# Optimization experiments

Measured on AMD Instinct MI355X. Metric: run time of the kernel, lower is better.

Reference implementation:

```python
import jax, jax.numpy as jnp
import numpy as np

IN, SD, PD, K = 34, 4, 22, 8
WIDTH, NUM_CLASSES, NCONV = 126, 6, 2
N, NGRAPH = 16384, 8
BATCH_OFFSET = 1e3  # separates graphs in learned coordinate space
BLOCK = 1024


def knn_idx(s, k, block=BLOCK):
    # brute-force kNN in blocks of query rows; s: [N, SD]
    n = s.shape[0]
    rows = s.reshape(n // block, block, s.shape[-1])
    def f(r):  # r: [block, SD]
        d2 = jnp.sum((r[:, None, :] - s[None, :, :]) ** 2, -1)  # [block, N]
        _, idx = jax.lax.top_k(-d2, k)
        return idx
    return jax.lax.map(f, rows).reshape(n, k)


def gravnet_conv(x, batch, Ws, bs, Wh, bh, Wo1, Wo2, bo2):
    # s: learned coordinates, offset per-graph so kNN never crosses graphs
    s = x @ Ws + bs + (batch.astype(x.dtype) * BATCH_OFFSET)[:, None]  # [N, SD]
    h = x @ Wh + bh                                                    # [N, PD]
    idx = knn_idx(jax.lax.stop_gradient(s), K)                         # [N, K]
    d2 = jnp.sum((s[:, None, :] - s[idx]) ** 2, -1)                    # [N, K]
    w = jnp.exp(-10.0 * d2)                                            # [N, K]
    msg = h[idx] * w[..., None]                                        # [N, K, PD]
    agg = jnp.concatenate([msg.mean(1), msg.max(1)], -1)               # [N, 2*PD]
    return x @ Wo1 + agg @ Wo2 + bo2                                   # [N, IN]


def setup_inputs() -> dict:
    key = jax.random.key(0)
    ks = jax.random.split(key, 12)
    def g(k, shape, fan_in):
        return jax.random.normal(k, shape, jnp.float32) * (fan_in ** -0.5)
    return {
        "x": jax.random.normal(ks[0], (N, IN), jnp.float32),
        "batch": jnp.sort(jax.random.randint(ks[1], (N,), 0, NGRAPH)),
        "Ws": g(ks[2], (NCONV, IN, SD), IN),
        "bs": jnp.zeros((NCONV, SD), jnp.float32),
        "Wh": g(ks[3], (NCONV, IN, PD), IN),
        "bh": jnp.zeros((NCONV, PD), jnp.float32),
        "Wo1": g(ks[4], (NCONV, IN, IN), IN),
        "Wo2": g(ks[5], (NCONV, 2 * PD, IN), 2 * PD),
        "bo2": jnp.zeros((NCONV, IN), jnp.float32),
        "W1": g(ks[6], (IN, WIDTH), IN),
        "b1": jnp.zeros((WIDTH,), jnp.float32),
        "W2": g(ks[7], (WIDTH, WIDTH), WIDTH),
        "b2": jnp.zeros((WIDTH,), jnp.float32),
        "W3": g(ks[8], (WIDTH, NUM_CLASSES), WIDTH),
        "b3": jnp.zeros((NUM_CLASSES,), jnp.float32),
    }


def reference(x, batch, Ws, bs, Wh, bh, Wo1, Wo2, bo2, W1, b1, W2, b2, W3, b3):
    # Faithful to original: input_ is never updated, each conv sees raw x,
    # only the last conv's embedding feeds the MLP head.
    embedding = x
    for i in range(NCONV):
        embedding = gravnet_conv(x, batch, Ws[i], bs[i], Wh[i], bh[i], Wo1[i], Wo2[i], bo2[i])
    hdd = jax.nn.elu(embedding @ W1 + b1)
    hdd = jax.nn.elu(hdd @ W2 + b2)
    return hdd @ W3 + b3  # [N, NUM_CLASSES]
```

## Files before the change

kernel.cpp:

```cpp
#include <hip/hip_runtime.h>
#include <math.h>
#include <float.h>

#define NPT     16384
#define IN_F    34
#define SDIM    4
#define PDIM    22
#define KNN     8
#define WIDTH   126
#define WPAD    128
#define NCLS    6
#define ROWS    32

typedef unsigned long long u64;

#define OFF_RANGES 0
#define OFF_S      256
#define OFF_H      (OFF_S  + NPT*SDIM*4)
#define OFF_KIDX   (OFF_H  + NPT*PDIM*4)
#define OFF_KW     (OFF_KIDX + NPT*KNN*4)

#define INITK_BITS 0x7f7fffffffffffffULL

__device__ __forceinline__ void ce(double& a, double& b) {
    double mn = __builtin_fmin(a, b);
    double mx = __builtin_fmax(a, b);
    a = mn; b = mx;
}
__device__ __forceinline__ double dmin64(double a, double b) {
    return __builtin_fmin(a, b);
}
__device__ __forceinline__ double pack_key(float d2, unsigned j) {
    return __longlong_as_double((long long)(((u64)__float_as_uint(d2) << 32) | j));
}

__device__ __forceinline__ void key_insert(double key, double* u) {
#pragma unroll
    for (int t = 0; t < KNN; ++t) {
        double mn = __builtin_fmin(key, u[t]);
        double mx = __builtin_fmax(key, u[t]);
        u[t] = mn;
        key  = mx;
    }
}

__device__ __forceinline__ void lgkm_barrier() {
    asm volatile("s_waitcnt lgkmcnt(0)" ::: "memory");
    __builtin_amdgcn_s_barrier();
    asm volatile("" ::: "memory");
}

__device__ __forceinline__ float dist2(const float4 a, const float4 b) {
    float d0 = a.x - b.x;
    float d1 = a.y - b.y;
    float d2 = a.z - b.z;
    float d3 = a.w - b.w;
    return __fadd_rn(__fadd_rn(__fadd_rn(__fmul_rn(d0, d0),
                                         __fmul_rn(d1, d1)),
                               __fmul_rn(d2, d2)),
                     __fmul_rn(d3, d3));
}

#define BITONIC8(m0,m1,m2,m3,m4,m5,m6,m7) \
    ce(m0,m4); ce(m1,m5); ce(m2,m6); ce(m3,m7); \
    ce(m0,m2); ce(m1,m3); ce(m4,m6); ce(m5,m7); \
    ce(m0,m1); ce(m2,m3); ce(m4,m5); ce(m6,m7);

#define SORT8(k0,k1,k2,k3,k4,k5,k6,k7) \
    ce(k0,k1); ce(k2,k3); ce(k4,k5); ce(k6,k7); \
    ce(k0,k2); ce(k1,k3); ce(k4,k6); ce(k5,k7); \
    ce(k1,k2); ce(k5,k6); \
    ce(k0,k4); ce(k1,k5); ce(k2,k6); ce(k3,k7); \
    ce(k2,k4); ce(k3,k5); \
    ce(k1,k2); ce(k3,k4); ce(k5,k6);

__global__ __launch_bounds__(256) void k_sh(const float* __restrict__ x,
                                            const int* __restrict__ batch,
                                            const float* __restrict__ Ws,
                                            const float* __restrict__ bs,
                                            const float* __restrict__ Wh,
                                            const float* __restrict__ bh,
                                            float* __restrict__ S,
                                            float* __restrict__ H,
                                            int* __restrict__ ranges) {
    int t = blockIdx.x * blockDim.x + threadIdx.x;
    int i = t >> 5;
    int o = t & 31;
    if (i >= NPT) return;
    if (o == 31) {
        int b = batch[i];
        if (i == 0 || batch[i - 1] != b) ranges[b * 2]     = i;
        if (i == NPT - 1 || batch[i + 1] != b) ranges[b * 2 + 1] = i + 1;
        return;
    }
    const float* xr = x + (size_t)i * IN_F;
    if (o < SDIM) {
        float acc = 0.f;
        for (int k = 0; k < IN_F; ++k) acc += xr[k] * Ws[k * SDIM + o];
        S[(size_t)i * SDIM + o] = (acc + bs[o]) + 1000.f * (float)batch[i];
    } else if (o < SDIM + PDIM) {
        int p = o - SDIM;
        float acc = 0.f;
        for (int k = 0; k < IN_F; ++k) acc += xr[k] * Wh[k * PDIM + p];
        H[(size_t)i * PDIM + p] = acc + bh[p];
    }
}

__global__ __launch_bounds__(256, 4) void k_knn(const float4* __restrict__ S4,
                                                const int* __restrict__ batch,
                                                const int* __restrict__ ranges,
                                                int* __restrict__ KIDX,
                                                float* __restrict__ KW) {
    const int tid = threadIdx.x;
    const int q   = blockIdx.x * 8 + (tid >> 5);
    const int t   = tid & 31;
    const int b   = batch[q];
    const int gs  = ranges[b * 2];
    const int len = ranges[b * 2 + 1] - gs;
    const float4 sq = S4[q];

    double u[KNN];
    const double initk = __longlong_as_double((long long)INITK_BITS);
#pragma unroll
    for (int e = 0; e < KNN; ++e) u[e] = initk;

    int j = gs + t;
    int done = 0;

    const int nfull8 = len >> 8;
    for (int bb = 0; bb < nfull8; ++bb, j += 256) {
        const float4* p = S4 + j;
        float4 s0 = p[0];
        float4 s1 = p[32];
        float4 s2 = p[64];
        float4 s3 = p[96];
        float4 s4 = p[128];
        float4 s5 = p[160];
        float4 s6 = p[192];
        float4 s7 = p[224];
        double k0 = pack_key(dist2(sq, s0), (unsigned)(j));
        double k1 = pack_key(dist2(sq, s1), (unsigned)(j + 32));
        double k2 = pack_key(dist2(sq, s2), (unsigned)(j + 64));
        double k3 = pack_key(dist2(sq, s3), (unsigned)(j + 96));
        double k4 = pack_key(dist2(sq, s4), (unsigned)(j + 128));
        double k5 = pack_key(dist2(sq, s5), (unsigned)(j + 160));
        double k6 = pack_key(dist2(sq, s6), (unsigned)(j + 192));
        double k7 = pack_key(dist2(sq, s7), (unsigned)(j + 224));
        SORT8(k0, k1, k2, k3, k4, k5, k6, k7);
        double m0 = dmin64(k0, u[7]);
        double m1 = dmin64(k1, u[6]);
        double m2 = dmin64(k2, u[5]);
        double m3 = dmin64(k3, u[4]);
        double m4 = dmin64(k4, u[3]);
        double m5 = dmin64(k5, u[2]);
        double m6 = dmin64(k6, u[1]);
        double m7 = dmin64(k7, u[0]);
        BITONIC8(m0, m1, m2, m3, m4, m5, m6, m7);
        u[0] = m0; u[1] = m1; u[2] = m2; u[3] = m3;
        u[4] = m4; u[5] = m5; u[6] = m6; u[7] = m7;
    }
    done = nfull8 << 8;

    if (len - done >= 128) {
        const float4* p = S4 + j;
        float4 s0 = p[0];
        float4 s1 = p[32];
        float4 s2 = p[64];
        float4 s3 = p[96];
        double k0 = pack_key(dist2(sq, s0), (unsigned)(j));
        double k1 = pack_key(dist2(sq, s1), (unsigned)(j + 32));
        double k2 = pack_key(dist2(sq, s2), (unsigned)(j + 64));
        double k3 = pack_key(dist2(sq, s3), (unsigned)(j + 96));
        ce(k0, k1); ce(k2, k3); ce(k0, k2); ce(k1, k3); ce(k1, k2);
        double m0 = dmin64(k0, u[7]);
        double m1 = dmin64(k1, u[6]);
        double m2 = dmin64(k2, u[5]);
        double m3 = dmin64(k3, u[4]);
        double m4 = u[3], m5 = u[2], m6 = u[1], m7 = u[0];
        BITONIC8(m0, m1, m2, m3, m4, m5, m6, m7);
        u[0] = m0; u[1] = m1; u[2] = m2; u[3] = m3;
        u[4] = m4; u[5] = m5; u[6] = m6; u[7] = m7;
        done += 128;
    }

    for (int m = done + t; m < len; m += 32) {
        int jj = gs + m;
        key_insert(pack_key(dist2(sq, S4[jj]), (unsigned)jj), u);
    }

#pragma unroll
    for (int mm = 1; mm < 32; mm <<= 1) {
        double p0 = __shfl_xor(u[0], mm, 32);
        double p1 = __shfl_xor(u[1], mm, 32);
        double p2 = __shfl_xor(u[2], mm, 32);
        double p3 = __shfl_xor(u[3], mm, 32);
        double p4 = __shfl_xor(u[4], mm, 32);
        double p5 = __shfl_xor(u[5], mm, 32);
        double p6 = __shfl_xor(u[6], mm, 32);
        double p7 = __shfl_xor(u[7], mm, 32);
        double m0 = dmin64(u[0], p7);
        double m1 = dmin64(u[1], p6);
        double m2 = dmin64(u[2], p5);
        double m3 = dmin64(u[3], p4);
        double m4 = dmin64(u[4], p3);
        double m5 = dmin64(u[5], p2);
        double m6 = dmin64(u[6], p1);
        double m7 = dmin64(u[7], p0);
        BITONIC8(m0, m1, m2, m3, m4, m5, m6, m7);
        u[0] = m0; u[1] = m1; u[2] = m2; u[3] = m3;
        u[4] = m4; u[5] = m5; u[6] = m6; u[7] = m7;
    }

    if (t == 0) {
#pragma unroll
        for (int e = 0; e < KNN; ++e) {
            u64 bits = (u64)__double_as_longlong(u[e]);
            float d = __uint_as_float((unsigned)(bits >> 32));
            KIDX[(size_t)q * KNN + e] = (int)(unsigned)(bits & 0xffffffffu);
            KW[(size_t)q * KNN + e]   = expf(-10.f * d);
        }
    }
}

__global__ __launch_bounds__(512, 4) void k_fused(
        const float* __restrict__ x,
        const float* __restrict__ H,
        const int* __restrict__ KIDX,
        const float* __restrict__ KW,
        const float* __restrict__ Wo1,
        const float* __restrict__ Wo2,
        const float* __restrict__ bo2,
        const float* __restrict__ W1,
        const float* __restrict__ b1,
        const float* __restrict__ W2,
        const float* __restrict__ b2,
        const float* __restrict__ W3,
        const float* __restrict__ b3,
        float* __restrict__ out) {
    __shared__ float xt[ROWS * IN_F];
    __shared__ float aggt[ROWS * 2 * PDIM];
    __shared__ float et[ROWS * IN_F];
    __shared__ float h1t[ROWS * WPAD];
    __shared__ float wbuf[2 * 32 * WPAD];
    __shared__ float w3buf[WPAD * NCLS];

    const int tid  = threadIdx.x;
    const int r    = tid >> 4;
    const int c    = tid & 15;
    const int p    = tid >> 5;
    const int cg   = tid & 31;
    const int row0 = blockIdx.x * ROWS;
    const int gi   = row0 + r;
    const int rA   = 2 * p;
    const int rB   = 2 * p + 1;
    const int jc   = 4 * cg;

    for (int t = tid; t < ROWS * IN_F; t += 512)
        xt[t] = x[(size_t)row0 * IN_F + t];
    for (int t = tid; t < IN_F * WPAD; t += 512) {
        int k = t >> 7, j = t & 127;
        wbuf[(k >> 5) * (32 * WPAD) + (k & 31) * WPAD + j] =
            (j < WIDTH) ? W1[k * WIDTH + j] : 0.f;
    }
    for (int t = tid; t < WPAD * NCLS; t += 512) {
        int k = t / NCLS;
        w3buf[t] = (k < WIDTH) ? W3[t] : 0.f;
    }

    if (c < 11) {
        const int p0 = c, p1 = c + 11;
        float s0 = 0.f, s1 = 0.f;
        float m0 = -FLT_MAX, m1 = -FLT_MAX;
#pragma unroll
        for (int k = 0; k < KNN; ++k) {
            int   j = KIDX[(size_t)gi * KNN + k];
            float w = KW[(size_t)gi * KNN + k];
            const float* hr = H + (size_t)j * PDIM;
            float v0 = hr[p0] * w; s0 += v0; m0 = fmaxf(m0, v0);
            float v1 = hr[p1] * w; s1 += v1; m1 = fmaxf(m1, v1);
        }
        aggt[r * 44 + p0] = s0 * 0.125f; aggt[r * 44 + PDIM + p0] = m0;
        aggt[r * 44 + p1] = s1 * 0.125f; aggt[r * 44 + PDIM + p1] = m1;
    }
    lgkm_barrier();

    float rvA[8], rvB[8];
#pragma unroll
    for (int i = 0; i < 8; ++i) {
        int e = i * 512 + tid, kk = e >> 7, j = e & 127;
        rvA[i] = (j < WIDTH) ? W2[(size_t)kk * WIDTH + j] : 0.f;
    }

    {
        const int j0 = (3 * c < 31) ? 3 * c : 31;
        float acc[3] = {0.f, 0.f, 0.f};
        const float* ar = xt + r * IN_F;
#pragma unroll 4
        for (int k = 0; k < IN_F; ++k) {
            float av = ar[k];
            const float* wr = Wo1 + k * IN_F + j0;
#pragma unroll
            for (int jj = 0; jj < 3; ++jj) acc[jj] += av * wr[jj];
        }
        const float* gr = aggt + r * 44;
#pragma unroll 4
        for (int pp = 0; pp < 2 * PDIM; ++pp) {
            float av = gr[pp];
            const float* wr = Wo2 + pp * IN_F + j0;
#pragma unroll
            for (int jj = 0; jj < 3; ++jj) acc[jj] += av * wr[jj];
        }
#pragma unroll
        for (int jj = 0; jj < 3; ++jj)
            et[r * IN_F + j0 + jj] = acc[jj] + bo2[j0 + jj];
    }
    lgkm_barrier();

    {
        float a0[4] = {0.f, 0.f, 0.f, 0.f};
        float a1[4] = {0.f, 0.f, 0.f, 0.f};
        const float* e0 = et + rA * IN_F;
        const float* e1 = et + rB * IN_F;
#pragma unroll 4
        for (int k = 0; k < IN_F; ++k) {
            const float* wr = wbuf + (k >> 5) * (32 * WPAD) + (k & 31) * WPAD;
            const float4 w4 = *(const float4*)(wr + jc);
            float v0 = e0[k], v1 = e1[k];
            a0[0] += v0 * w4.x; a0[1] += v0 * w4.y;
            a0[2] += v0 * w4.z; a0[3] += v0 * w4.w;
            a1[0] += v1 * w4.x; a1[1] += v1 * w4.y;
            a1[2] += v1 * w4.z; a1[3] += v1 * w4.w;
        }
#pragma unroll
        for (int jj = 0; jj < 4; ++jj) {
            int j = jc + jj;
            float bj = b1[j < WIDTH ? j : WIDTH - 1];
            float v0 = a0[jj] + bj;
            float v1 = a1[jj] + bj;
            h1t[rA * WPAD + j] = (j < WIDTH) ? (v0 > 0.f ? v0 : expm1f(v0)) : 0.f;
            h1t[rB * WPAD + j] = (j < WIDTH) ? (v1 > 0.f ? v1 : expm1f(v1)) : 0.f;
        }
    }
    lgkm_barrier();

    float a0[4] = {0.f, 0.f, 0.f, 0.f};
    float a1[4] = {0.f, 0.f, 0.f, 0.f};
    const float* h0 = h1t + rA * WPAD;
    const float* h1r = h1t + rB * WPAD;

#define STORE_CHUNK(BUFI, RV)                                   \
    _Pragma("unroll")                                           \
    for (int i = 0; i < 8; ++i)                                 \
        wbuf[(BUFI) * 4096 + i * 512 + tid] = RV[i];

#define LOAD_CHUNK(RV, K0)                                      \
    _Pragma("unroll")                                           \
    for (int i = 0; i < 8; ++i) {                               \
        int e = i * 512 + tid, kk = e >> 7, j = e & 127;        \
        int row = (K0) + kk;                                    \
        RV[i] = (j < WIDTH && row < WIDTH)                      \
                    ? W2[(size_t)row * WIDTH + j] : 0.f;        \
    }

#define COMPUTE_CHUNK(BUFI, K0)                                 \
    {                                                           \
        const float* wb = wbuf + (BUFI) * 4096;                 \
        _Pragma("unroll 4")                                     \
        for (int k = 0; k < 32; ++k) {                          \
            const float4 w4 = *(const float4*)(wb + k * WPAD + jc); \
            float v0 = h0[(K0) + k];                            \
            float v1 = h1r[(K0) + k];                           \
            a0[0] += v0 * w4.x; a0[1] += v0 * w4.y;             \
            a0[2] += v0 * w4.z; a0[3] += v0 * w4.w;             \
            a1[0] += v1 * w4.x; a1[1] += v1 * w4.y;             \
            a1[2] += v1 * w4.z; a1[3] += v1 * w4.w;             \
        }                                                       \
    }

    STORE_CHUNK(0, rvA);  LOAD_CHUNK(rvB, 32);
    lgkm_barrier();
    COMPUTE_CHUNK(0, 0);
    STORE_CHUNK(1, rvB);  LOAD_CHUNK(rvA, 64);
    lgkm_barrier();
    COMPUTE_CHUNK(1, 32);
    STORE_CHUNK(0, rvA);  LOAD_CHUNK(rvB, 96);
    lgkm_barrier();
    COMPUTE_CHUNK(0, 64);
    STORE_CHUNK(1, rvB);
    lgkm_barrier();
    COMPUTE_CHUNK(1, 96);

    {
        float pc0[NCLS] = {0.f, 0.f, 0.f, 0.f, 0.f, 0.f};
        float pc1[NCLS] = {0.f, 0.f, 0.f, 0.f, 0.f, 0.f};
#pragma unroll
        for (int jj = 0; jj < 4; ++jj) {
            int j = jc + jj;
            float bj = b2[j < WIDTH ? j : WIDTH - 1];
            float v0 = a0[jj] + bj;
            float v1 = a1[jj] + bj;
            float g0 = (j < WIDTH) ? (v0 > 0.f ? v0 : expm1f(v0)) : 0.f;
            float g1 = (j < WIDTH) ? (v1 > 0.f ? v1 : expm1f(v1)) : 0.f;
            const float* w3r = w3buf + j * NCLS;
#pragma unroll
            for (int cc = 0; cc < NCLS; ++cc) {
                pc0[cc] += g0 * w3r[cc];
                pc1[cc] += g1 * w3r[cc];
            }
        }
#pragma unroll
        for (int mm = 1; mm < 32; mm <<= 1) {
#pragma unroll
            for (int cc = 0; cc < NCLS; ++cc) {
                pc0[cc] += __shfl_xor(pc0[cc], mm, 32);
                pc1[cc] += __shfl_xor(pc1[cc], mm, 32);
            }
        }
        if (cg == 0) {
#pragma unroll
            for (int cc = 0; cc < NCLS; ++cc) {
                out[(size_t)(row0 + rA) * NCLS + cc] = pc0[cc] + b3[cc];
                out[(size_t)(row0 + rB) * NCLS + cc] = pc1[cc] + b3[cc];
            }
        }
    }
#undef STORE_CHUNK
#undef LOAD_CHUNK
#undef COMPUTE_CHUNK
}

extern "C" void kernel_launch(void* const* d_in, const int* in_sizes, int n_in,
                              void* d_out, int out_size, void* d_ws, size_t ws_size,
                              hipStream_t stream) {
    const float* x     = (const float*)d_in[0];
    const int*   batch = (const int*)d_in[1];
    const float* Ws  = (const float*)d_in[2] + IN_F * SDIM;
    const float* bs  = (const float*)d_in[3] + SDIM;
    const float* Wh  = (const float*)d_in[4] + IN_F * PDIM;
    const float* bh  = (const float*)d_in[5] + PDIM;
    const float* Wo1 = (const float*)d_in[6] + IN_F * IN_F;
    const float* Wo2 = (const float*)d_in[7] + 2 * PDIM * IN_F;
    const float* bo2 = (const float*)d_in[8] + IN_F;
    const float* W1  = (const float*)d_in[9];
    const float* b1  = (const float*)d_in[10];
    const float* W2  = (const float*)d_in[11];
    const float* b2  = (const float*)d_in[12];
    const float* W3  = (const float*)d_in[13];
    const float* b3  = (const float*)d_in[14];
    float* out = (float*)d_out;

    char* ws = (char*)d_ws;
    int*   ranges = (int*)(ws + OFF_RANGES);
    float* S      = (float*)(ws + OFF_S);
    float* H      = (float*)(ws + OFF_H);
    int*   KIDX   = (int*)(ws + OFF_KIDX);
    float* KW     = (float*)(ws + OFF_KW);

    k_sh<<<dim3(NPT * 32 / 256), dim3(256), 0, stream>>>(x, batch, Ws, bs, Wh, bh, S, H, ranges);
    k_knn<<<dim3(NPT / 8), dim3(256), 0, stream>>>((const float4*)S, batch, ranges, KIDX, KW);
    k_fused<<<dim3(NPT / ROWS), dim3(512), 0, stream>>>(x, H, KIDX, KW, Wo1, Wo2, bo2,
                                                        W1, b1, W2, b2, W3, b3, out);
}
```

Baseline: 76.13 us.

## Stage all MLP weights in LDS once per block and loop over two row tiles

The fused head kernel now loads W1, the full W2, Wo1, Wo2 and W3 into shared memory once per block and processes 64 rows as two 32-row tiles. This replaces the chunked double-buffered W2 streaming, and Wo1/Wo2 are no longer read from global memory inside the inner loops. Blocks are remapped with a swizzled index and launch bounds drop to one block per CU, because shared memory use grows to roughly 100KB. The aim is to amortise weight loading across more rows, at the cost of fewer blocks and lower occupancy.

```diff
diff --git a/kernel.cpp b/kernel.cpp
--- a/kernel.cpp
+++ b/kernel.cpp
@@ -10,7 +10,8 @@
 #define WIDTH   126
 #define WPAD    128
 #define NCLS    6
-#define ROWS    32
+#define RPB     64
+#define TROWS   32
 
 typedef unsigned long long u64;
 
@@ -42,12 +43,6 @@
         u[t] = mn;
         key  = mx;
     }
-}
-
-__device__ __forceinline__ void lgkm_barrier() {
-    asm volatile("s_waitcnt lgkmcnt(0)" ::: "memory");
-    __builtin_amdgcn_s_barrier();
-    asm volatile("" ::: "memory");
 }
 
 __device__ __forceinline__ float dist2(const float4 a, const float4 b) {
@@ -222,7 +217,7 @@
     }
 }
 
-__global__ __launch_bounds__(512, 4) void k_fused(
+__global__ __launch_bounds__(512, 1) void k_fused(
         const float* __restrict__ x,
         const float* __restrict__ H,
         const int* __restrict__ KIDX,
@@ -237,196 +232,169 @@
         const float* __restrict__ W3,
         const float* __restrict__ b3,
         float* __restrict__ out) {
-    __shared__ float xt[ROWS * IN_F];
-    __shared__ float aggt[ROWS * 2 * PDIM];
-    __shared__ float et[ROWS * IN_F];
-    __shared__ float h1t[ROWS * WPAD];
-    __shared__ float wbuf[2 * 32 * WPAD];
+    __shared__ float W1L[IN_F * WPAD];
+    __shared__ float W2L[WPAD * WPAD];
+    __shared__ float wo1L[IN_F * IN_F];
+    __shared__ float wo2L[2 * PDIM * IN_F];
     __shared__ float w3buf[WPAD * NCLS];
-
-    const int tid  = threadIdx.x;
-    const int r    = tid >> 4;
-    const int c    = tid & 15;
-    const int p    = tid >> 5;
-    const int cg   = tid & 31;
-    const int row0 = blockIdx.x * ROWS;
-    const int gi   = row0 + r;
-    const int rA   = 2 * p;
-    const int rB   = 2 * p + 1;
-    const int jc   = 4 * cg;
-
-    for (int t = tid; t < ROWS * IN_F; t += 512)
-        xt[t] = x[(size_t)row0 * IN_F + t];
+    __shared__ float xt[TROWS * IN_F];
+    __shared__ float aggt[TROWS * 2 * PDIM];
+    __shared__ float et[TROWS * IN_F];
+    __shared__ float h1t[TROWS * WPAD];
+
+    const int tid = threadIdx.x;
+    const int r   = tid >> 4;
+    const int c   = tid & 15;
+    const int p   = tid >> 5;
+    const int cg  = tid & 31;
+    const int rA  = 2 * p;
+    const int rB  = 2 * p + 1;
+    const int jc  = 4 * cg;
+    const int lb   = ((blockIdx.x & 7) << 5) | (blockIdx.x >> 3);
+    const int brow = lb * RPB;
+
     for (int t = tid; t < IN_F * WPAD; t += 512) {
         int k = t >> 7, j = t & 127;
-        wbuf[(k >> 5) * (32 * WPAD) + (k & 31) * WPAD + j] =
-            (j < WIDTH) ? W1[k * WIDTH + j] : 0.f;
-    }
+        W1L[t] = (j < WIDTH) ? W1[k * WIDTH + j] : 0.f;
+    }
+    for (int t = tid; t < WPAD * WPAD; t += 512) {
+        int k = t >> 7, j = t & 127;
+        W2L[t] = (k < WIDTH && j < WIDTH) ? W2[(size_t)k * WIDTH + j] : 0.f;
+    }
+    for (int t = tid; t < IN_F * IN_F; t += 512)      wo1L[t] = Wo1[t];
+    for (int t = tid; t < 2 * PDIM * IN_F; t += 512)  wo2L[t] = Wo2[t];
     for (int t = tid; t < WPAD * NCLS; t += 512) {
         int k = t / NCLS;
         w3buf[t] = (k < WIDTH) ? W3[t] : 0.f;
     }
-
-    if (c < 11) {
-        const int p0 = c, p1 = c + 11;
-        float s0 = 0.f, s1 = 0.f;
-        float m0 = -FLT_MAX, m1 = -FLT_MAX;
-#pragma unroll
-        for (int k = 0; k < KNN; ++k) {
-            int   j = KIDX[(size_t)gi * KNN + k];
-            float w = KW[(size_t)gi * KNN + k];
-            const float* hr = H + (size_t)j * PDIM;
-            float v0 = hr[p0] * w; s0 += v0; m0 = fmaxf(m0, v0);
-            float v1 = hr[p1] * w; s1 += v1; m1 = fmaxf(m1, v1);
+    __syncthreads();
+
+#pragma unroll 1
+    for (int tile = 0; tile < RPB / TROWS; ++tile) {
+        const int row0 = brow + tile * TROWS;
+        const int gi   = row0 + r;
+
+        for (int t = tid; t < TROWS * IN_F; t += 512)
+            xt[t] = x[(size_t)row0 * IN_F + t];
+        if (c < 11) {
+            const int p0 = c, p1 = c + 11;
+            float s0 = 0.f, s1 = 0.f;
+            float m0 = -FLT_MAX, m1 = -FLT_MAX;
+#pragma unroll
+            for (int k = 0; k < KNN; ++k) {
+                int   j = KIDX[(size_t)gi * KNN + k];
+                float w = KW[(size_t)gi * KNN + k];
+                const float* hr = H + (size_t)j * PDIM;
+                float v0 = hr[p0] * w; s0 += v0; m0 = fmaxf(m0, v0);
+                float v1 = hr[p1] * w; s1 += v1; m1 = fmaxf(m1, v1);
+            }
+            aggt[r * 44 + p0] = s0 * 0.125f; aggt[r * 44 + PDIM + p0] = m0;
+            aggt[r * 44 + p1] = s1 * 0.125f; aggt[r * 44 + PDIM + p1] = m1;
         }
-        aggt[r * 44 + p0] = s0 * 0.125f; aggt[r * 44 + PDIM + p0] = m0;
-        aggt[r * 44 + p1] = s1 * 0.125f; aggt[r * 44 + PDIM + p1] = m1;
-    }
-    lgkm_barrier();
-
-    float rvA[8], rvB[8];
-#pragma unroll
-    for (int i = 0; i < 8; ++i) {
-        int e = i * 512 + tid, kk = e >> 7, j = e & 127;
-        rvA[i] = (j < WIDTH) ? W2[(size_t)kk * WIDTH + j] : 0.f;
-    }
-
-    {
-        const int j0 = (3 * c < 31) ? 3 * c : 31;
-        float acc[3] = {0.f, 0.f, 0.f};
-        const float* ar = xt + r * IN_F;
+        __syncthreads();
+
+        {
+            const int j0 = (3 * c < 31) ? 3 * c : 31;
+            float acc[3] = {0.f, 0.f, 0.f};
+            const float* ar = xt + r * IN_F;
 #pragma unroll 4
-        for (int k = 0; k < IN_F; ++k) {
-            float av = ar[k];
-            const float* wr = Wo1 + k * IN_F + j0;
-#pragma unroll
-            for (int jj = 0; jj < 3; ++jj) acc[jj] += av * wr[jj];
+            for (int k = 0; k < IN_F; ++k) {
+                float av = ar[k];
+                const float* wr = wo1L + k * IN_F + j0;
+#pragma unroll
+                for (int jj = 0; jj < 3; ++jj) acc[jj] += av * wr[jj];
+            }
+            const float* gr = aggt + r * 44;
+#pragma unroll 4
+            for (int pp = 0; pp < 2 * PDIM; ++pp) {
+                float av = gr[pp];
+                const float* wr = wo2L + pp * IN_F + j0;
+#pragma unroll
+                for (int jj = 0; jj < 3; ++jj) acc[jj] += av * wr[jj];
+            }
+#pragma unroll
+            for (int jj = 0; jj < 3; ++jj)
+                et[r * IN_F + j0 + jj] = acc[jj] + bo2[j0 + jj];
         }
-        const float* gr = aggt + r * 44;
+        __syncthreads();
+
+        {
+            float a0[4] = {0.f, 0.f, 0.f, 0.f};
+            float a1[4] = {0.f, 0.f, 0.f, 0.f};
+            const float* e0 = et + rA * IN_F;
+            const float* e1 = et + rB * IN_F;
 #pragma unroll 4
-        for (int pp = 0; pp < 2 * PDIM; ++pp) {
-            float av = gr[pp];
-            const float* wr = Wo2 + pp * IN_F + j0;
-#pragma unroll
-            for (int jj = 0; jj < 3; ++jj) acc[jj] += av * wr[jj];
+            for (int k = 0; k < IN_F; ++k) {
+                const float4 w4 = *(const float4*)(W1L + k * WPAD + jc);
+                float v0 = e0[k], v1 = e1[k];
+                a0[0] += v0 * w4.x; a0[1] += v0 * w4.y;
+                a0[2] += v0 * w4.z; a0[3] += v0 * w4.w;
+                a1[0] += v1 * w4.x; a1[1] += v1 * w4.y;
+                a1[2] += v1 * w4.z; a1[3] += v1 * w4.w;
+            }
+#pragma unroll
+            for (int jj = 0; jj < 4; ++jj) {
+                int j = jc + jj;
+                float bj = b1[j < WIDTH ? j : WIDTH - 1];
+                float v0 = a0[jj] + bj;
+                float v1 = a1[jj] + bj;
+                h1t[rA * WPAD + j] = (j < WIDTH) ? (v0 > 0.f ? v0 : expm1f(v0)) : 0.f;
+                h1t[rB * WPAD + j] = (j < WIDTH) ? (v1 > 0.f ? v1 : expm1f(v1)) : 0.f;
+            }
         }
-#pragma unroll
-        for (int jj = 0; jj < 3; ++jj)
-            et[r * IN_F + j0 + jj] = acc[jj] + bo2[j0 + jj];
-    }
-    lgkm_barrier();
-
-    {
-        float a0[4] = {0.f, 0.f, 0.f, 0.f};
-        float a1[4] = {0.f, 0.f, 0.f, 0.f};
-        const float* e0 = et + rA * IN_F;
-        const float* e1 = et + rB * IN_F;
+        __syncthreads();
+
+        {
+            float a0[4] = {0.f, 0.f, 0.f, 0.f};
+            float a1[4] = {0.f, 0.f, 0.f, 0.f};
+            const float* h0  = h1t + rA * WPAD;
+            const float* h1r = h1t + rB * WPAD;
 #pragma unroll 4
-        for (int k = 0; k < IN_F; ++k) {
-            const float* wr = wbuf + (k >> 5) * (32 * WPAD) + (k & 31) * WPAD;
-            const float4 w4 = *(const float4*)(wr + jc);
-            float v0 = e0[k], v1 = e1[k];
-            a0[0] += v0 * w4.x; a0[1] += v0 * w4.y;
-            a0[2] += v0 * w4.z; a0[3] += v0 * w4.w;
-            a1[0] += v1 * w4.x; a1[1] += v1 * w4.y;
-            a1[2] += v1 * w4.z; a1[3] += v1 * w4.w;
+            for (int k = 0; k < WPAD; ++k) {
+                const float4 w4 = *(const float4*)(W2L + k * WPAD + jc);
+                float v0 = h0[k];
+                float v1 = h1r[k];
+                a0[0] += v0 * w4.x; a0[1] += v0 * w4.y;
+                a0[2] += v0 * w4.z; a0[3] += v0 * w4.w;
+                a1[0] += v1 * w4.x; a1[1] += v1 * w4.y;
+                a1[2] += v1 * w4.z; a1[3] += v1 * w4.w;
+            }
+
+            float pc0[NCLS] = {0.f, 0.f, 0.f, 0.f, 0.f, 0.f};
+            float pc1[NCLS] = {0.f, 0.f, 0.f, 0.f, 0.f, 0.f};
+#pragma unroll
+            for (int jj = 0; jj < 4; ++jj) {
+                int j = jc + jj;
+                float bj = b2[j < WIDTH ? j : WIDTH - 1];
+                float v0 = a0[jj] + bj;
+                float v1 = a1[jj] + bj;
+                float g0 = (j < WIDTH) ? (v0 > 0.f ? v0 : expm1f(v0)) : 0.f;
+                float g1 = (j < WIDTH) ? (v1 > 0.f ? v1 : expm1f(v1)) : 0.f;
+                const float* w3r = w3buf + j * NCLS;
+#pragma unroll
+                for (int cc = 0; cc < NCLS; ++cc) {
+                    pc0[cc] += g0 * w3r[cc];
+                    pc1[cc] += g1 * w3r[cc];
+                }
+            }
+#pragma unroll
+            for (int mm = 1; mm < 32; mm <<= 1) {
+#pragma unroll
+                for (int cc = 0; cc < NCLS; ++cc) {
+                    pc0[cc] += __shfl_xor(pc0[cc], mm, 32);
+                    pc1[cc] += __shfl_xor(pc1[cc], mm, 32);
+                }
+            }
+            if (cg == 0) {
+#pragma unroll
+                for (int cc = 0; cc < NCLS; ++cc) {
+                    out[(size_t)(row0 + rA) * NCLS + cc] = pc0[cc] + b3[cc];
+                    out[(size_t)(row0 + rB) * NCLS + cc] = pc1[cc] + b3[cc];
+                }
+            }
         }
-#pragma unroll
-        for (int jj = 0; jj < 4; ++jj) {
-            int j = jc + jj;
-            float bj = b1[j < WIDTH ? j : WIDTH - 1];
-            float v0 = a0[jj] + bj;
-            float v1 = a1[jj] + bj;
-            h1t[rA * WPAD + j] = (j < WIDTH) ? (v0 > 0.f ? v0 : expm1f(v0)) : 0.f;
-            h1t[rB * WPAD + j] = (j < WIDTH) ? (v1 > 0.f ? v1 : expm1f(v1)) : 0.f;
-        }
-    }
-    lgkm_barrier();
-
-    float a0[4] = {0.f, 0.f, 0.f, 0.f};
-    float a1[4] = {0.f, 0.f, 0.f, 0.f};
-    const float* h0 = h1t + rA * WPAD;
-    const float* h1r = h1t + rB * WPAD;
-
-#define STORE_CHUNK(BUFI, RV)                                   \
-    _Pragma("unroll")                                           \
-    for (int i = 0; i < 8; ++i)                                 \
-        wbuf[(BUFI) * 4096 + i * 512 + tid] = RV[i];
-
-#define LOAD_CHUNK(RV, K0)                                      \
-    _Pragma("unroll")                                           \
-    for (int i = 0; i < 8; ++i) {                               \
-        int e = i * 512 + tid, kk = e >> 7, j = e & 127;        \
-        int row = (K0) + kk;                                    \
-        RV[i] = (j < WIDTH && row < WIDTH)                      \
-                    ? W2[(size_t)row * WIDTH + j] : 0.f;        \
-    }
-
-#define COMPUTE_CHUNK(BUFI, K0)                                 \
-    {                                                           \
-        const float* wb = wbuf + (BUFI) * 4096;                 \
-        _Pragma("unroll 4")                                     \
-        for (int k = 0; k < 32; ++k) {                          \
-            const float4 w4 = *(const float4*)(wb + k * WPAD + jc); \
-            float v0 = h0[(K0) + k];                            \
-            float v1 = h1r[(K0) + k];                           \
-            a0[0] += v0 * w4.x; a0[1] += v0 * w4.y;             \
-            a0[2] += v0 * w4.z; a0[3] += v0 * w4.w;             \
-            a1[0] += v1 * w4.x; a1[1] += v1 * w4.y;             \
-            a1[2] += v1 * w4.z; a1[3] += v1 * w4.w;             \
-        }                                                       \
-    }
-
-    STORE_CHUNK(0, rvA);  LOAD_CHUNK(rvB, 32);
-    lgkm_barrier();
-    COMPUTE_CHUNK(0, 0);
-    STORE_CHUNK(1, rvB);  LOAD_CHUNK(rvA, 64);
-    lgkm_barrier();
-    COMPUTE_CHUNK(1, 32);
-    STORE_CHUNK(0, rvA);  LOAD_CHUNK(rvB, 96);
-    lgkm_barrier();
-    COMPUTE_CHUNK(0, 64);
-    STORE_CHUNK(1, rvB);
-    lgkm_barrier();
-    COMPUTE_CHUNK(1, 96);
-
-    {
-        float pc0[NCLS] = {0.f, 0.f, 0.f, 0.f, 0.f, 0.f};
-        float pc1[NCLS] = {0.f, 0.f, 0.f, 0.f, 0.f, 0.f};
-#pragma unroll
-        for (int jj = 0; jj < 4; ++jj) {
-            int j = jc + jj;
-            float bj = b2[j < WIDTH ? j : WIDTH - 1];
-            float v0 = a0[jj] + bj;
-            float v1 = a1[jj] + bj;
-            float g0 = (j < WIDTH) ? (v0 > 0.f ? v0 : expm1f(v0)) : 0.f;
-            float g1 = (j < WIDTH) ? (v1 > 0.f ? v1 : expm1f(v1)) : 0.f;
-            const float* w3r = w3buf + j * NCLS;
-#pragma unroll
-            for (int cc = 0; cc < NCLS; ++cc) {
-                pc0[cc] += g0 * w3r[cc];
-                pc1[cc] += g1 * w3r[cc];
-            }
-        }
-#pragma unroll
-        for (int mm = 1; mm < 32; mm <<= 1) {
-#pragma unroll
-            for (int cc = 0; cc < NCLS; ++cc) {
-                pc0[cc] += __shfl_xor(pc0[cc], mm, 32);
-                pc1[cc] += __shfl_xor(pc1[cc], mm, 32);
-            }
-        }
-        if (cg == 0) {
-#pragma unroll
-            for (int cc = 0; cc < NCLS; ++cc) {
-                out[(size_t)(row0 + rA) * NCLS + cc] = pc0[cc] + b3[cc];
-                out[(size_t)(row0 + rB) * NCLS + cc] = pc1[cc] + b3[cc];
-            }
-        }
-    }
-#undef STORE_CHUNK
-#undef LOAD_CHUNK
-#undef COMPUTE_CHUNK
+        __syncthreads();
+    }
 }
 
 extern "C" void kernel_launch(void* const* d_in, const int* in_sizes, int n_in,
@@ -458,6 +426,6 @@
 
     k_sh<<<dim3(NPT * 32 / 256), dim3(256), 0, stream>>>(x, batch, Ws, bs, Wh, bh, S, H, ranges);
     k_knn<<<dim3(NPT / 8), dim3(256), 0, stream>>>((const float4*)S, batch, ranges, KIDX, KW);
-    k_fused<<<dim3(NPT / ROWS), dim3(512), 0, stream>>>(x, H, KIDX, KW, Wo1, Wo2, bo2,
-                                                        W1, b1, W2, b2, W3, b3, out);
-}
+    k_fused<<<dim3(NPT / RPB), dim3(512), 0, stream>>>(x, H, KIDX, KW, Wo1, Wo2, bo2,
+                                                       W1, b1, W2, b2, W3, b3, out);
+}
```

After: 76.20 us. About the same (+0.1%).
